# Performance work log

Measured on AMD Instinct MI355X. Metric: run time of the kernel, lower is better.

## Reference

```python
import jax, jax.numpy as jnp
import numpy as np

CONF_THRES = 0.25   # NMS.conf
IOU_THRES = 0.45    # NMS.iou
MAX_NMS = 1024      # fixed candidate count so greedy NMS is jit-compatible
IMG = 640.0


def setup_inputs() -> dict:
    key = jax.random.key(0)
    k0, k1, k2, k3, k4 = jax.random.split(key, 5)
    B, N = 32, 25200
    cxcy = jax.random.uniform(k0, (B, N, 2), dtype=jnp.float32) * IMG
    wh = jax.random.uniform(k1, (B, N, 2), dtype=jnp.float32) * 80.0 + 2.0
    obj = jax.random.uniform(k2, (B, N, 1), dtype=jnp.float32)
    lmk = jax.random.uniform(k3, (B, N, 10), dtype=jnp.float32) * IMG
    cls = jax.random.uniform(k4, (B, N, 1), dtype=jnp.float32)
    # layout: [cx, cy, w, h, obj, 10 landmark coords, 1 class score]
    prediction = jnp.concatenate([cxcy, wh, obj, lmk, cls], axis=2)
    return {"prediction": prediction}


def xywh2xyxy(x):
    cx, cy, w, h = x[:, 0], x[:, 1], x[:, 2], x[:, 3]
    return jnp.stack([cx - w / 2, cy - h / 2, cx + w / 2, cy + h / 2], axis=1)


def pairwise_iou(b):  # b: [K,4] xyxy -> [K,K]
    area = (b[:, 2] - b[:, 0]) * (b[:, 3] - b[:, 1])
    lt = jnp.maximum(b[:, None, :2], b[None, :, :2])
    rb = jnp.minimum(b[:, None, 2:], b[None, :, 2:])
    wh = jnp.clip(rb - lt, 0.0)
    inter = wh[..., 0] * wh[..., 1]
    return inter / (area[:, None] + area[None, :] - inter + 1e-7)


def _nms_image(pred):  # pred: [N,16]
    obj = pred[:, 4]
    score = pred[:, 15] * obj  # x[:,15:] *= x[:,4:5]; nc==1 -> single class, j==0
    valid = (obj > CONF_THRES) & (score > CONF_THRES)  # xc filter + conf filter
    s = jnp.where(valid, score, -1.0)
    top_s, idx = jax.lax.top_k(s, MAX_NMS)  # score-sorted candidates (greedy NMS order)
    x = pred[idx]  # [K,16]
    box = xywh2xyxy(x[:, :4])
    vmask = top_s > 0.0  # valid candidates (invalid slots carry score -1)
    # class offset c = j*4096 is identically 0 since nc==1 -> skip
    iou = pairwise_iou(box)  # [K,K]
    rng = jnp.arange(MAX_NMS)

    def step(keep, i):
        sup = keep[i] & (iou[i] > IOU_THRES) & (rng > i)
        return keep & ~sup, None

    keep, _ = jax.lax.scan(step, vmask, rng)
    det = jnp.concatenate(
        [box, top_s[:, None], x[:, 5:15], jnp.zeros((MAX_NMS, 1), pred.dtype)], axis=1
    )  # [K,16] = box(4) | conf(1) | landmarks(10) | class(1)=0
    return det * keep[:, None].astype(det.dtype), keep


def reference(prediction):
    # Fixed-shape analogue of the per-image ragged output: detections padded to
    # MAX_NMS rows per image (zeroed where suppressed) plus a keep mask.
    det, keep = jax.vmap(_nms_image)(prediction)
    return det, keep
```

## Files before the change

kernel.cpp:

```cpp
#include <hip/hip_runtime.h>
#include <stdint.h>

#define NB 32
#define NN 25200
#define NN4 6300
#define TOPK 1024
#define NF 16
#define CONF 0.25f
#define IOU_T 0.45f
#define NBIN 4096
#define CAP 2048
#define KEY_BASE 0xBE800001u

__device__ __forceinline__ uint32_t score_key(float obj, float cls) {
  float score = __fmul_rn(cls, obj);
  bool valid = (obj > CONF) && (score > CONF);
  float s = valid ? score : -1.0f;
  uint32_t u = __float_as_uint(s);
  return (u & 0x80000000u) ? ~u : (u | 0x80000000u);
}

__device__ __forceinline__ uint64_t shfl_xor_u64(uint64_t v, int m) {
  uint32_t lo = __shfl_xor((uint32_t)v, m, 64);
  uint32_t hi = __shfl_xor((uint32_t)(v >> 32), m, 64);
  return ((uint64_t)hi << 32) | lo;
}

__global__ void k_keys(const float* __restrict__ pred, uint32_t* __restrict__ keys) {
  int g = blockIdx.x * blockDim.x + threadIdx.x;
  if (g >= NB * NN) return;
  const float* row = pred + (size_t)g * NF;
  keys[g] = score_key(row[4], row[15]);
}

__global__ __launch_bounds__(1024) void k_select(const uint32_t* __restrict__ keys,
                                                 int* __restrict__ sel) {
  int b = blockIdx.x;
  int tid = threadIdx.x;
  int lane = tid & 63, wid = tid >> 6;
  const uint32_t* kb = keys + (size_t)b * NN;
  const uint4* kb4 = (const uint4*)kb;
  __shared__ uint32_t hist[NBIN];
  __shared__ uint64_t ent[CAP];
  __shared__ uint32_t wsum[16];
  __shared__ uint32_t sh_bin;
  __shared__ uint32_t sh_cnt;
  #pragma unroll
  for (int k = 0; k < 4; ++k) hist[tid + 1024 * k] = 0;
  ent[tid] = 0; ent[tid + 1024] = 0;
  if (tid == 0) { sh_cnt = 0; sh_bin = 0; }
  __syncthreads();

  for (int i = tid; i < NN4; i += 1024) {
    uint4 k4 = kb4[i];
    uint32_t kv[4] = {k4.x, k4.y, k4.z, k4.w};
    #pragma unroll
    for (int c = 0; c < 4; ++c) {
      uint32_t key = kv[c];
      if (key >= KEY_BASE) {
        uint32_t bin = (key - KEY_BASE) >> 12;
        if (bin > NBIN - 1) bin = NBIN - 1;
        atomicAdd(&hist[bin], 1u);
      }
    }
  }
  __syncthreads();

  uint32_t h[4]; uint32_t s = 0;
  #pragma unroll
  for (int k = 0; k < 4; ++k) { h[k] = hist[NBIN - 1 - (4 * tid + k)]; s += h[k]; }
  uint32_t my = s;
  #pragma unroll
  for (int d = 1; d < 64; d <<= 1) {
    uint32_t v = __shfl_up(s, d, 64);
    if (lane >= d) s += v;
  }
  if (lane == 63) wsum[wid] = s;
  __syncthreads();
  uint32_t base = 0;
  for (int w = 0; w < wid; ++w) base += wsum[w];
  uint32_t cum = base + s - my;
  #pragma unroll
  for (int k = 0; k < 4; ++k) {
    if (cum < TOPK && cum + h[k] >= TOPK) sh_bin = (uint32_t)(NBIN - 1 - (4 * tid + k));
    cum += h[k];
  }
  __syncthreads();
  uint32_t thr = KEY_BASE + (sh_bin << 12);

  for (int i = tid; i < NN4; i += 1024) {
    uint4 k4 = kb4[i];
    uint32_t kv[4] = {k4.x, k4.y, k4.z, k4.w};
    #pragma unroll
    for (int c = 0; c < 4; ++c) {
      uint32_t key = kv[c];
      if (key >= thr) {
        uint32_t p = atomicAdd(&sh_cnt, 1u);
        if (p < CAP) ent[p] = ((uint64_t)key << 32) | (uint32_t)(~(uint32_t)(4 * i + c));
      }
    }
  }
  __syncthreads();

  uint64_t v0 = ent[tid], v1 = ent[tid + 1024];
  for (unsigned kk = 2; kk <= CAP; kk <<= 1) {
    for (unsigned j = kk >> 1; j > 0; j >>= 1) {
      if (j == 1024) {
        uint64_t mx = v0 > v1 ? v0 : v1;
        uint64_t mn = v0 > v1 ? v1 : v0;
        v0 = mx; v1 = mn;
      } else if (j >= 64) {
        __syncthreads();
        ent[tid] = v0; ent[tid + 1024] = v1;
        __syncthreads();
        uint64_t p0 = ent[tid ^ j], p1 = ent[(tid ^ j) + 1024];
        bool low = ((tid & j) == 0);
        bool d0 = ((tid & kk) == 0);
        bool d1 = (((tid + 1024) & kk) == 0);
        v0 = (low != d0) ? (v0 < p0 ? v0 : p0) : (v0 > p0 ? v0 : p0);
        v1 = (low != d1) ? (v1 < p1 ? v1 : p1) : (v1 > p1 ? v1 : p1);
      } else {
        uint64_t p0 = shfl_xor_u64(v0, (int)j);
        uint64_t p1 = shfl_xor_u64(v1, (int)j);
        bool low = ((tid & j) == 0);
        bool d0 = ((tid & kk) == 0);
        bool d1 = (((tid + 1024) & kk) == 0);
        v0 = (low != d0) ? (v0 < p0 ? v0 : p0) : (v0 > p0 ? v0 : p0);
        v1 = (low != d1) ? (v1 < p1 ? v1 : p1) : (v1 > p1 ? v1 : p1);
      }
    }
  }
  uint32_t n = ~(uint32_t)(v0 & 0xFFFFFFFFu);
  if (n >= NN) n = 0;
  sel[(size_t)b * TOPK + tid] = (int)n;
}

__global__ __launch_bounds__(1024) void k_mask(const float* __restrict__ pred,
                                               const int* __restrict__ sel,
                                               uint32_t* __restrict__ mask) {
  int b = blockIdx.x;
  int sblk = blockIdx.y;
  int tid = threadIdx.x;
  int r_local = tid & 127;
  int part = tid >> 7;
  int i = sblk * 128 + r_local;
  if (part < sblk) {
    #pragma unroll
    for (int wN = 0; wN < 4; ++wN)
      mask[(size_t)b * (32 * TOPK) + (size_t)(part * 4 + wN) * TOPK + i] = 0u;
  }
  __shared__ float bx1[TOPK], by1[TOPK], bx2[TOPK], by2[TOPK], bar[TOPK];
  {
    int n = sel[(size_t)b * TOPK + tid];
    const float4* row = (const float4*)(pred + ((size_t)b * NN + n) * NF);
    float4 r0 = row[0];
    float hw = __fmul_rn(r0.z, 0.5f), hh = __fmul_rn(r0.w, 0.5f);
    float x1 = __fsub_rn(r0.x, hw), y1 = __fsub_rn(r0.y, hh);
    float x2 = __fadd_rn(r0.x, hw), y2 = __fadd_rn(r0.y, hh);
    bx1[tid] = x1; by1[tid] = y1; bx2[tid] = x2; by2[tid] = y2;
    bar[tid] = __fmul_rn(__fsub_rn(x2, x1), __fsub_rn(y2, y1));
  }
  __syncthreads();
  if (part < sblk) return;
  float x1i = bx1[i], y1i = by1[i], x2i = bx2[i], y2i = by2[i], ai = bar[i];
  int jbase = part * 128;
  for (int wN = 0; wN < 4; ++wN) {
    uint32_t word = 0;
    int j0 = jbase + wN * 32;
    #pragma unroll
    for (int t2 = 0; t2 < 32; ++t2) {
      int j = j0 + t2;
      float lx = fmaxf(x1i, bx1[j]);
      float ly = fmaxf(y1i, by1[j]);
      float rx = fminf(x2i, bx2[j]);
      float ry = fminf(y2i, by2[j]);
      float wd = fmaxf(__fsub_rn(rx, lx), 0.0f);
      float ht = fmaxf(__fsub_rn(ry, ly), 0.0f);
      float inter = __fmul_rn(wd, ht);
      float den = __fadd_rn(__fsub_rn(__fadd_rn(ai, bar[j]), inter), 1e-7f);
      float iou = __fdiv_rn(inter, den);
      uint32_t bit = ((iou > IOU_T) && (j > i)) ? 1u : 0u;
      word |= bit << t2;
    }
    mask[(size_t)b * (32 * TOPK) + (size_t)(part * 4 + wN) * TOPK + i] = word;
  }
}

__global__ __launch_bounds__(1024) void k_scan_out(const float* __restrict__ pred,
                                                   const int* __restrict__ sel,
                                                   const uint32_t* __restrict__ mask,
                                                   float* __restrict__ det,
                                                   float* __restrict__ keep_out) {
  int b = blockIdx.x;
  int tid = threadIdx.x;
  int lane = tid & 63, wv = tid >> 6;
  __shared__ uint32_t vbits[32];
  __shared__ uint32_t keepw[32];

  int n = sel[(size_t)b * TOPK + tid];
  const float4* rowv = (const float4*)(pred + ((size_t)b * NN + n) * NF);
  float4 r0 = rowv[0], r1 = rowv[1], r2 = rowv[2], r3 = rowv[3];
  float obj = r1.x, cls = r3.w;
  float score = __fmul_rn(cls, obj);
  bool valid = (obj > CONF) && (score > CONF);
  uint64_t bal = __ballot(valid);
  if (lane == 0) {
    vbits[2 * wv] = (uint32_t)bal;
    vbits[2 * wv + 1] = (uint32_t)(bal >> 32);
  }
  __syncthreads();

  if (tid < 32) {
    int l = tid;
    uint32_t kw = vbits[l];
    const uint4* mc = (const uint4*)(mask + (size_t)b * (32 * TOPK) + (size_t)l * TOPK);
    uint32_t cur[32], nxt[32];
    #pragma unroll
    for (int q = 0; q < 8; ++q) *(uint4*)&cur[4 * q] = mc[q];
    for (int w = 0; w < 32; ++w) {
      if (w < 31) {
        #pragma unroll
        for (int q = 0; q < 8; ++q) *(uint4*)&nxt[4 * q] = mc[(w + 1) * 8 + q];
      }
      uint32_t rw = kw;
      #pragma unroll
      for (int t = 0; t < 32; ++t)
        if ((rw >> t) & 1u) rw &= ~cur[t];
      uint32_t rf = __shfl(rw, w, 64);
      if (l == w) {
        kw = rf;
      } else {
        #pragma unroll
        for (int t = 0; t < 32; ++t)
          if ((rf >> t) & 1u) kw &= ~cur[t];
      }
      if (w < 31) {
        #pragma unroll
        for (int t = 0; t < 32; ++t) cur[t] = nxt[t];
      }
    }
    keepw[l] = kw;
  }
  __syncthreads();

  bool kept = (keepw[tid >> 5] >> (tid & 31)) & 1u;
  float m = kept ? 1.0f : 0.0f;
  float hw = __fmul_rn(r0.z, 0.5f), hh = __fmul_rn(r0.w, 0.5f);
  float4 o0 = make_float4(__fsub_rn(r0.x, hw) * m, __fsub_rn(r0.y, hh) * m,
                          __fadd_rn(r0.x, hw) * m, __fadd_rn(r0.y, hh) * m);
  float4 o1 = make_float4(score * m, r1.y * m, r1.z * m, r1.w * m);
  float4 o2 = make_float4(r2.x * m, r2.y * m, r2.z * m, r2.w * m);
  float4 o3 = make_float4(r3.x * m, r3.y * m, r3.z * m, 0.0f);
  float4* dst = (float4*)(det + ((size_t)b * TOPK + tid) * NF);
  dst[0] = o0; dst[1] = o1; dst[2] = o2; dst[3] = o3;
  keep_out[(size_t)b * TOPK + tid] = m;
}

extern "C" void kernel_launch(void* const* d_in, const int* in_sizes, int n_in,
                              void* d_out, int out_size, void* d_ws, size_t ws_size,
                              hipStream_t stream) {
  const float* pred = (const float*)d_in[0];
  float* det = (float*)d_out;
  float* keep = det + (size_t)NB * TOPK * NF;

  uint8_t* ws = (uint8_t*)d_ws;
  uint32_t* keys = (uint32_t*)ws;
  int* sel = (int*)(ws + (size_t)NB * NN * 4);
  uint32_t* mask = (uint32_t*)(ws + (size_t)NB * NN * 4
                                  + (size_t)NB * TOPK * 4);

  k_keys<<<(NB * NN + 255) / 256, 256, 0, stream>>>(pred, keys);
  k_select<<<NB, 1024, 0, stream>>>(keys, sel);
  dim3 gm(NB, 8);
  k_mask<<<gm, 1024, 0, stream>>>(pred, sel, mask);
  k_scan_out<<<NB, 1024, 0, stream>>>(pred, sel, mask, det, keep);
}
```

Before: 172.8 us.

## Fuse IoU mask build and greedy scan into one kernel using LDS mask

Merges the separate IoU bitmask kernel and the scan/output kernel into a single per-image kernel. The suppression bitmask is kept in padded shared memory instead of a global workspace, and box corners are computed once and reused for the output. This removes a kernel launch and the global mask write and read. In exchange, the mask computation runs on only one block per image rather than eight. The triangular work is also split unevenly across threads, and the large LDS footprint limits occupancy.

```diff
diff --git a/kernel.cpp b/kernel.cpp
--- a/kernel.cpp
+++ b/kernel.cpp
@@ -11,6 +11,7 @@
 #define NBIN 4096
 #define CAP 2048
 #define KEY_BASE 0xBE800001u
+#define MSTRIDE 33
 
 __device__ __forceinline__ uint32_t score_key(float obj, float cls) {
   float score = __fmul_rn(cls, obj);
@@ -135,67 +136,17 @@
   sel[(size_t)b * TOPK + tid] = (int)n;
 }
 
-__global__ __launch_bounds__(1024) void k_mask(const float* __restrict__ pred,
-                                               const int* __restrict__ sel,
-                                               uint32_t* __restrict__ mask) {
-  int b = blockIdx.x;
-  int sblk = blockIdx.y;
-  int tid = threadIdx.x;
-  int r_local = tid & 127;
-  int part = tid >> 7;
-  int i = sblk * 128 + r_local;
-  if (part < sblk) {
-    #pragma unroll
-    for (int wN = 0; wN < 4; ++wN)
-      mask[(size_t)b * (32 * TOPK) + (size_t)(part * 4 + wN) * TOPK + i] = 0u;
-  }
+__global__ __launch_bounds__(1024) void k_nms(const float* __restrict__ pred,
+                                              const int* __restrict__ sel,
+                                              float* __restrict__ det,
+                                              float* __restrict__ keep_out) {
   __shared__ float bx1[TOPK], by1[TOPK], bx2[TOPK], by2[TOPK], bar[TOPK];
-  {
-    int n = sel[(size_t)b * TOPK + tid];
-    const float4* row = (const float4*)(pred + ((size_t)b * NN + n) * NF);
-    float4 r0 = row[0];
-    float hw = __fmul_rn(r0.z, 0.5f), hh = __fmul_rn(r0.w, 0.5f);
-    float x1 = __fsub_rn(r0.x, hw), y1 = __fsub_rn(r0.y, hh);
-    float x2 = __fadd_rn(r0.x, hw), y2 = __fadd_rn(r0.y, hh);
-    bx1[tid] = x1; by1[tid] = y1; bx2[tid] = x2; by2[tid] = y2;
-    bar[tid] = __fmul_rn(__fsub_rn(x2, x1), __fsub_rn(y2, y1));
-  }
-  __syncthreads();
-  if (part < sblk) return;
-  float x1i = bx1[i], y1i = by1[i], x2i = bx2[i], y2i = by2[i], ai = bar[i];
-  int jbase = part * 128;
-  for (int wN = 0; wN < 4; ++wN) {
-    uint32_t word = 0;
-    int j0 = jbase + wN * 32;
-    #pragma unroll
-    for (int t2 = 0; t2 < 32; ++t2) {
-      int j = j0 + t2;
-      float lx = fmaxf(x1i, bx1[j]);
-      float ly = fmaxf(y1i, by1[j]);
-      float rx = fminf(x2i, bx2[j]);
-      float ry = fminf(y2i, by2[j]);
-      float wd = fmaxf(__fsub_rn(rx, lx), 0.0f);
-      float ht = fmaxf(__fsub_rn(ry, ly), 0.0f);
-      float inter = __fmul_rn(wd, ht);
-      float den = __fadd_rn(__fsub_rn(__fadd_rn(ai, bar[j]), inter), 1e-7f);
-      float iou = __fdiv_rn(inter, den);
-      uint32_t bit = ((iou > IOU_T) && (j > i)) ? 1u : 0u;
-      word |= bit << t2;
-    }
-    mask[(size_t)b * (32 * TOPK) + (size_t)(part * 4 + wN) * TOPK + i] = word;
-  }
-}
-
-__global__ __launch_bounds__(1024) void k_scan_out(const float* __restrict__ pred,
-                                                   const int* __restrict__ sel,
-                                                   const uint32_t* __restrict__ mask,
-                                                   float* __restrict__ det,
-                                                   float* __restrict__ keep_out) {
+  __shared__ uint32_t lmask[TOPK * MSTRIDE];
+  __shared__ uint32_t vbits[32];
+  __shared__ uint32_t keepw[32];
   int b = blockIdx.x;
   int tid = threadIdx.x;
   int lane = tid & 63, wv = tid >> 6;
-  __shared__ uint32_t vbits[32];
-  __shared__ uint32_t keepw[32];
 
   int n = sel[(size_t)b * TOPK + tid];
   const float4* rowv = (const float4*)(pred + ((size_t)b * NN + n) * NF);
@@ -208,35 +159,61 @@
     vbits[2 * wv] = (uint32_t)bal;
     vbits[2 * wv + 1] = (uint32_t)(bal >> 32);
   }
+  float hw = __fmul_rn(r0.z, 0.5f), hh = __fmul_rn(r0.w, 0.5f);
+  float x1i = __fsub_rn(r0.x, hw), y1i = __fsub_rn(r0.y, hh);
+  float x2i = __fadd_rn(r0.x, hw), y2i = __fadd_rn(r0.y, hh);
+  float ai = __fmul_rn(__fsub_rn(x2i, x1i), __fsub_rn(y2i, y1i));
+  bx1[tid] = x1i; by1[tid] = y1i; bx2[tid] = x2i; by2[tid] = y2i; bar[tid] = ai;
+  __syncthreads();
+
+  {
+    int i = tid;
+    int w0 = i >> 5;
+    uint32_t lowmask = (2u << (i & 31)) - 1u;
+    for (int w = w0; w < 32; ++w) {
+      uint32_t word = 0;
+      #pragma unroll
+      for (int t = 0; t < 32; ++t) {
+        int j = w * 32 + t;
+        float lx = fmaxf(x1i, bx1[j]);
+        float ly = fmaxf(y1i, by1[j]);
+        float rx = fminf(x2i, bx2[j]);
+        float ry = fminf(y2i, by2[j]);
+        float wd = fmaxf(__fsub_rn(rx, lx), 0.0f);
+        float ht = fmaxf(__fsub_rn(ry, ly), 0.0f);
+        float inter = __fmul_rn(wd, ht);
+        float den = __fadd_rn(__fsub_rn(__fadd_rn(ai, bar[j]), inter), 1e-7f);
+        float iou = __fdiv_rn(inter, den);
+        word |= (iou > IOU_T ? 1u : 0u) << t;
+      }
+      if (w == w0) word &= ~lowmask;
+      lmask[i * MSTRIDE + w] = word;
+    }
+  }
   __syncthreads();
 
   if (tid < 32) {
     int l = tid;
     uint32_t kw = vbits[l];
-    const uint4* mc = (const uint4*)(mask + (size_t)b * (32 * TOPK) + (size_t)l * TOPK);
-    uint32_t cur[32], nxt[32];
-    #pragma unroll
-    for (int q = 0; q < 8; ++q) *(uint4*)&cur[4 * q] = mc[q];
     for (int w = 0; w < 32; ++w) {
-      if (w < 31) {
+      uint32_t rf;
+      if (l >= w) {
+        uint32_t cur[32];
         #pragma unroll
-        for (int q = 0; q < 8; ++q) *(uint4*)&nxt[4 * q] = mc[(w + 1) * 8 + q];
-      }
-      uint32_t rw = kw;
-      #pragma unroll
-      for (int t = 0; t < 32; ++t)
-        if ((rw >> t) & 1u) rw &= ~cur[t];
-      uint32_t rf = __shfl(rw, w, 64);
-      if (l == w) {
-        kw = rf;
-      } else {
+        for (int t = 0; t < 32; ++t) cur[t] = lmask[(w * 32 + t) * MSTRIDE + l];
+        uint32_t rw = kw;
         #pragma unroll
         for (int t = 0; t < 32; ++t)
-          if ((rf >> t) & 1u) kw &= ~cur[t];
-      }
-      if (w < 31) {
-        #pragma unroll
-        for (int t = 0; t < 32; ++t) cur[t] = nxt[t];
+          if ((rw >> t) & 1u) rw &= ~cur[t];
+        rf = __shfl(rw, w, 64);
+        if (l == w) {
+          kw = rf;
+        } else {
+          uint32_t acc = 0;
+          #pragma unroll
+          for (int t = 0; t < 32; ++t) acc |= ((rf >> t) & 1u) ? cur[t] : 0u;
+          kw &= ~acc;
+        }
       }
     }
     keepw[l] = kw;
@@ -245,9 +222,7 @@
 
   bool kept = (keepw[tid >> 5] >> (tid & 31)) & 1u;
   float m = kept ? 1.0f : 0.0f;
-  float hw = __fmul_rn(r0.z, 0.5f), hh = __fmul_rn(r0.w, 0.5f);
-  float4 o0 = make_float4(__fsub_rn(r0.x, hw) * m, __fsub_rn(r0.y, hh) * m,
-                          __fadd_rn(r0.x, hw) * m, __fadd_rn(r0.y, hh) * m);
+  float4 o0 = make_float4(x1i * m, y1i * m, x2i * m, y2i * m);
   float4 o1 = make_float4(score * m, r1.y * m, r1.z * m, r1.w * m);
   float4 o2 = make_float4(r2.x * m, r2.y * m, r2.z * m, r2.w * m);
   float4 o3 = make_float4(r3.x * m, r3.y * m, r3.z * m, 0.0f);
@@ -266,12 +241,8 @@
   uint8_t* ws = (uint8_t*)d_ws;
   uint32_t* keys = (uint32_t*)ws;
   int* sel = (int*)(ws + (size_t)NB * NN * 4);
-  uint32_t* mask = (uint32_t*)(ws + (size_t)NB * NN * 4
-                                  + (size_t)NB * TOPK * 4);
 
   k_keys<<<(NB * NN + 255) / 256, 256, 0, stream>>>(pred, keys);
   k_select<<<NB, 1024, 0, stream>>>(keys, sel);
-  dim3 gm(NB, 8);
-  k_mask<<<gm, 1024, 0, stream>>>(pred, sel, mask);
-  k_scan_out<<<NB, 1024, 0, stream>>>(pred, sel, mask, det, keep);
-}
+  k_nms<<<NB, 1024, 0, stream>>>(pred, sel, det, keep);
+}
```

Result: slower. 281.4 us (+62.9%).

## Remap IoU mask threads to column-words with 4-row register tiles and vector stores

Applied to the files above, without the earlier changes.

The mask kernel now assigns each thread one 32-column word for four consecutive rows. Column boxes are read from shared memory once and reused across the four rows held in registers, and the four words are written with a single uint4 store. The j>i check is replaced by a bitmask applied only to the diagonal word, and below-diagonal words are written as zeros by the same store. The scan kernel skips suppression updates for lanes below the current word, uses a branchless OR accumulation, and gets a launch_bounds occupancy hint. The per-thread work becomes more uneven across column groups, and the larger register tile may raise register pressure.

```diff
diff --git a/kernel.cpp b/kernel.cpp
--- a/kernel.cpp
+++ b/kernel.cpp
@@ -141,14 +141,8 @@
   int b = blockIdx.x;
   int sblk = blockIdx.y;
   int tid = threadIdx.x;
-  int r_local = tid & 127;
-  int part = tid >> 7;
-  int i = sblk * 128 + r_local;
-  if (part < sblk) {
-    #pragma unroll
-    for (int wN = 0; wN < 4; ++wN)
-      mask[(size_t)b * (32 * TOPK) + (size_t)(part * 4 + wN) * TOPK + i] = 0u;
-  }
+  int rg = tid & 31;
+  int cc = tid >> 5;
   __shared__ float bx1[TOPK], by1[TOPK], bx2[TOPK], by2[TOPK], bar[TOPK];
   {
     int n = sel[(size_t)b * TOPK + tid];
@@ -161,36 +155,48 @@
     bar[tid] = __fmul_rn(__fsub_rn(x2, x1), __fsub_rn(y2, y1));
   }
   __syncthreads();
-  if (part < sblk) return;
-  float x1i = bx1[i], y1i = by1[i], x2i = bx2[i], y2i = by2[i], ai = bar[i];
-  int jbase = part * 128;
-  for (int wN = 0; wN < 4; ++wN) {
-    uint32_t word = 0;
-    int j0 = jbase + wN * 32;
-    #pragma unroll
-    for (int t2 = 0; t2 < 32; ++t2) {
-      int j = j0 + t2;
-      float lx = fmaxf(x1i, bx1[j]);
-      float ly = fmaxf(y1i, by1[j]);
-      float rx = fminf(x2i, bx2[j]);
-      float ry = fminf(y2i, by2[j]);
-      float wd = fmaxf(__fsub_rn(rx, lx), 0.0f);
-      float ht = fmaxf(__fsub_rn(ry, ly), 0.0f);
-      float inter = __fmul_rn(wd, ht);
-      float den = __fadd_rn(__fsub_rn(__fadd_rn(ai, bar[j]), inter), 1e-7f);
-      float iou = __fdiv_rn(inter, den);
-      uint32_t bit = ((iou > IOU_T) && (j > i)) ? 1u : 0u;
-      word |= bit << t2;
-    }
-    mask[(size_t)b * (32 * TOPK) + (size_t)(part * 4 + wN) * TOPK + i] = word;
-  }
-}
-
-__global__ __launch_bounds__(1024) void k_scan_out(const float* __restrict__ pred,
-                                                   const int* __restrict__ sel,
-                                                   const uint32_t* __restrict__ mask,
-                                                   float* __restrict__ det,
-                                                   float* __restrict__ keep_out) {
+  int i0 = sblk * 128 + rg * 4;
+  int iw = i0 >> 5;
+  uint32_t wreg[4] = {0u, 0u, 0u, 0u};
+  if (cc >= iw) {
+    float rx1[4], ry1[4], rx2[4], ry2[4], rar[4];
+    #pragma unroll
+    for (int k = 0; k < 4; ++k) {
+      rx1[k] = bx1[i0 + k]; ry1[k] = by1[i0 + k];
+      rx2[k] = bx2[i0 + k]; ry2[k] = by2[i0 + k]; rar[k] = bar[i0 + k];
+    }
+    for (int jj = 0; jj < 32; ++jj) {
+      int j = cc * 32 + jj;
+      float cx1 = bx1[j], cy1 = by1[j], cx2 = bx2[j], cy2 = by2[j], car = bar[j];
+      #pragma unroll
+      for (int k = 0; k < 4; ++k) {
+        float lx = fmaxf(rx1[k], cx1);
+        float ly = fmaxf(ry1[k], cy1);
+        float rx = fminf(rx2[k], cx2);
+        float ry = fminf(ry2[k], cy2);
+        float wd = fmaxf(__fsub_rn(rx, lx), 0.0f);
+        float ht = fmaxf(__fsub_rn(ry, ly), 0.0f);
+        float inter = __fmul_rn(wd, ht);
+        float den = __fadd_rn(__fsub_rn(__fadd_rn(rar[k], car), inter), 1e-7f);
+        float iou = __fdiv_rn(inter, den);
+        wreg[k] |= (iou > IOU_T ? 1u : 0u) << jj;
+      }
+    }
+    if (cc == iw) {
+      #pragma unroll
+      for (int k = 0; k < 4; ++k)
+        wreg[k] &= ~((2u << ((i0 + k) & 31)) - 1u);
+    }
+  }
+  uint4 out = make_uint4(wreg[0], wreg[1], wreg[2], wreg[3]);
+  *(uint4*)&mask[((size_t)b * 32 + cc) * TOPK + i0] = out;
+}
+
+__global__ __launch_bounds__(1024, 4) void k_scan_out(const float* __restrict__ pred,
+                                                      const int* __restrict__ sel,
+                                                      const uint32_t* __restrict__ mask,
+                                                      float* __restrict__ det,
+                                                      float* __restrict__ keep_out) {
   int b = blockIdx.x;
   int tid = threadIdx.x;
   int lane = tid & 63, wv = tid >> 6;
@@ -229,10 +235,11 @@
       uint32_t rf = __shfl(rw, w, 64);
       if (l == w) {
         kw = rf;
-      } else {
+      } else if (l > w) {
+        uint32_t acc = 0;
         #pragma unroll
-        for (int t = 0; t < 32; ++t)
-          if ((rf >> t) & 1u) kw &= ~cur[t];
+        for (int t = 0; t < 32; ++t) acc |= ((rf >> t) & 1u) ? cur[t] : 0u;
+        kw &= ~acc;
       }
       if (w < 31) {
         #pragma unroll
```

Measured after the change: 167.6 us. 3.0% less time.
